# Kernel tuning notes

Measured on AMD Instinct MI355X. Metric: run time of the kernel, lower is better.

Reference implementation:

```python
import jax, jax.numpy as jnp
import numpy as np

B, S = 512, 64
ZD, GD, SK = 256, 16, 512   # vel_z_dim, genre_cond_dim, skel_encode_dim
H = 1024                    # vel_hidden_dim
ND, VC = 9, 4               # n_drum_classes, vel_cond_dim


def _gru(x, h, Wi, Wh, bi, bh):
    # torch.nn.GRUCell math; gates ordered [r, z, n]
    gi = x @ Wi.T + bi
    gh = h @ Wh.T + bh
    i_r, i_z, i_n = jnp.split(gi, 3, axis=-1)
    h_r, h_z, h_n = jnp.split(gh, 3, axis=-1)
    r = jax.nn.sigmoid(i_r + h_r)
    zg = jax.nn.sigmoid(i_z + h_z)
    n = jnp.tanh(i_n + r * h_n)
    return (1.0 - zg) * n + zg * h


def setup_inputs() -> dict:
    key = jax.random.key(0)
    ks = jax.random.split(key, 14)
    rn = lambda k, shp, s: jax.random.normal(k, shp, dtype=jnp.float32) * s
    return dict(
        z=rn(ks[0], (B, ZD), 1.0),
        note_encoded=rn(ks[1], (B, SK), 1.0),
        vel_target=jax.random.uniform(ks[2], (B, S, ND), dtype=jnp.float32),
        note=jax.random.uniform(ks[3], (B, S, ND), dtype=jnp.float32),
        vel_cond=jax.random.uniform(ks[4], (B, S, VC), dtype=jnp.float32),
        genre_cond=rn(ks[5], (B, GD), 1.0),
        W_in=rn(ks[6], (H, ZD + SK + GD), 0.02), b_in=jnp.zeros((H,), jnp.float32),
        W_ih1=rn(ks[7], (3 * H, ND * 2 + VC), 0.05), W_hh1=rn(ks[8], (3 * H, H), 0.02),
        b_ih1=jnp.zeros((3 * H,), jnp.float32), b_hh1=jnp.zeros((3 * H,), jnp.float32),
        W_ih2=rn(ks[9], (3 * H, H), 0.02), W_hh2=rn(ks[10], (3 * H, H), 0.02),
        b_ih2=jnp.zeros((3 * H,), jnp.float32), b_hh2=jnp.zeros((3 * H,), jnp.float32),
        W_out=rn(ks[11], (ND, H), 0.02), b_out=jnp.zeros((ND,), jnp.float32),
        training=0, teacher_forcing_ratio=0,
    )


def reference(z, note_encoded, vel_target, note, vel_cond, genre_cond,
              W_in, b_in, W_ih1, W_hh1, b_ih1, b_hh1,
              W_ih2, W_hh2, b_ih2, b_hh2, W_out, b_out,
              training, teacher_forcing_ratio):
    # eval mode: dropout = identity, teacher forcing never taken
    del vel_target, training, teacher_forcing_ratio
    bsz = z.shape[0]
    zc = jnp.concatenate([z.reshape(bsz, -1), note_encoded, genre_cond], axis=-1)
    h1 = jnp.tanh(zc @ W_in.T + b_in)              # [B, H]
    h2 = jnp.zeros_like(h1)                        # overwritten at step 0
    out0 = jnp.zeros((bsz, W_out.shape[0]), z.dtype)

    def step(carry, xs):
        out, h1, h2 = carry
        i, nt, ct = xs
        inp = jnp.concatenate([out, nt, ct], axis=-1)       # [B, 2*ND+VC]
        h1 = _gru(inp, h1, W_ih1, W_hh1, b_ih1, b_hh1)
        h2 = jnp.where(i == 0, h1, h2)                      # hx[1] = hx[0] at i==0
        h2 = _gru(h1, h2, W_ih2, W_hh2, b_ih2, b_hh2)
        vel = jax.nn.sigmoid(h2 @ W_out.T + b_out)          # [B, ND]
        return (vel, h1, h2), vel

    xs = (jnp.arange(note.shape[1]),
          jnp.transpose(note, (1, 0, 2)),
          jnp.transpose(vel_cond, (1, 0, 2)))
    _, outs = jax.lax.scan(step, (out0, h1, h2), xs)
    return jnp.transpose(outs, (1, 0, 2))                    # [B, S, ND]
```

## Files before the change

kernel.cpp:

```cpp
#include <hip/hip_runtime.h>
#include <hip/hip_bf16.h>

#define HD 1024
#define BB 512
#define SS 64
#define N3 3072
#define NC 9216
#define ND 9
#define VC 4
#define KI 832

typedef __attribute__((ext_vector_type(8))) short bf16x8;
typedef __attribute__((ext_vector_type(4))) float f32x4;

__device__ __forceinline__ ushort f2b(float f) {
    unsigned u = __builtin_bit_cast(unsigned, f);
    u += 0x7fffu + ((u >> 16) & 1u);
    return (ushort)(u >> 16);
}

__device__ __forceinline__ float b2f(ushort u) {
    unsigned x = ((unsigned)u) << 16;
    return __builtin_bit_cast(float, x);
}

__device__ __forceinline__ float sigf(float x) {
    return 1.f / (1.f + __expf(-x));
}

__device__ __forceinline__ void gld_lds16(const void* g, void* l) {
    __builtin_amdgcn_global_load_lds(
        (const __attribute__((address_space(1))) unsigned int*)g,
        (__attribute__((address_space(3))) unsigned int*)l, 16, 0, 0);
}

__global__ __launch_bounds__(256) void prep_w(
    const float* __restrict__ Wih2, const float* __restrict__ Whh1,
    const float* __restrict__ Whh2, ushort* __restrict__ Wcat)
{
    const int row = blockIdx.x;
    const float* src = row < 3072 ? Wih2 + (size_t)row * HD
                     : row < 6144 ? Whh1 + (size_t)(row - 3072) * HD
                                  : Whh2 + (size_t)(row - 6144) * HD;
    const int c = threadIdx.x * 4;
    float4 v = *(const float4*)(src + c);
    ushort4 o;
    o.x = f2b(v.x); o.y = f2b(v.y); o.z = f2b(v.z); o.w = f2b(v.w);
    *(ushort4*)(Wcat + (size_t)row * HD + c) = o;
}

__global__ __launch_bounds__(256) void prep_wt1(
    const float* __restrict__ Wih1, ushort* __restrict__ Wt1b)
{
    const int g = blockIdx.x * 256 + threadIdx.x;
    #pragma unroll
    for (int c = 0; c < 22; ++c)
        Wt1b[c * N3 + g] = f2b(Wih1[(size_t)g * 22 + c]);
}

__global__ __launch_bounds__(256) void prep_acat(
    const float* __restrict__ z, const float* __restrict__ ne,
    const float* __restrict__ gc, ushort* __restrict__ Acat)
{
    const int b = blockIdx.x;
    const int t = threadIdx.x;
    if (t >= 208) return;
    const int c = t * 4;
    float4 v = make_float4(0.f, 0.f, 0.f, 0.f);
    if (c < 256)      v = *(const float4*)(z  + (size_t)b * 256 + c);
    else if (c < 768) v = *(const float4*)(ne + (size_t)b * 512 + (c - 256));
    else if (c < 784) v = *(const float4*)(gc + (size_t)b * 16  + (c - 768));
    ushort4 o;
    o.x = f2b(v.x); o.y = f2b(v.y); o.z = f2b(v.z); o.w = f2b(v.w);
    *(ushort4*)(Acat + (size_t)b * KI + c) = o;
}

__global__ __launch_bounds__(256) void prep_win(
    const float* __restrict__ W_in, ushort* __restrict__ W_inb)
{
    const int r = blockIdx.x;
    const int t = threadIdx.x;
    if (t >= 208) return;
    const int c = t * 4;
    ushort4 o = {0, 0, 0, 0};
    if (c < 784) {
        float4 v = *(const float4*)(W_in + (size_t)r * 784 + c);
        o.x = f2b(v.x); o.y = f2b(v.y); o.z = f2b(v.z); o.w = f2b(v.w);
    }
    *(ushort4*)(W_inb + (size_t)r * KI + c) = o;
}

__global__ __launch_bounds__(256) void k_init(
    const ushort* __restrict__ Acat, const ushort* __restrict__ W_inb,
    const float* __restrict__ b_in, float* __restrict__ h1, ushort* __restrict__ h1b)
{
    __shared__ __align__(16) ushort As[2 * 4096];
    __shared__ __align__(16) ushort Bs[2 * 4096];
    const int t = blockIdx.x;
    const int nt = t >> 3, mt = t & 7;

    const int tid = threadIdx.x;
    const int w = tid >> 6, l = tid & 63;
    const int lr = l >> 3;
    const int sw = ((l & 7) ^ lr) << 3;

    const ushort* Ag0 = Acat + ((size_t)(mt << 6) + 16 * w + lr) * KI + sw;
    const ushort* Ag1 = Ag0 + 8 * KI;
    const ushort* Bg0 = W_inb + ((size_t)(nt << 6) + 16 * w + lr) * KI + sw;
    const ushort* Bg1 = Bg0 + 8 * KI;
    const int o0 = (16 * w) * 64, o1 = (16 * w + 8) * 64;

    gld_lds16(Ag0, As + o0); gld_lds16(Ag1, As + o1);
    gld_lds16(Bg0, Bs + o0); gld_lds16(Bg1, Bs + o1);

    const int wm = (w >> 1) << 5, wn = (w & 1) << 5;
    const int fr = l & 15, fc = l >> 4;
    const int ra0 = wm + fr, ra1 = wm + 16 + fr;
    const int rb0 = wn + fr, rb1 = wn + 16 + fr;

    f32x4 acc[2][2] = {};
    for (int kt = 0; kt < 13; ++kt) {
        const int cb = (kt & 1) << 12;
        __syncthreads();
        if (kt + 1 < 13) {
            const int nb = ((kt + 1) & 1) << 12;
            const int ko = (kt + 1) << 6;
            gld_lds16(Ag0 + ko, As + nb + o0);
            gld_lds16(Ag1 + ko, As + nb + o1);
            gld_lds16(Bg0 + ko, Bs + nb + o0);
            gld_lds16(Bg1 + ko, Bs + nb + o1);
        }
        #pragma unroll
        for (int kk = 0; kk < 2; ++kk) {
            const int c = (kk << 2) + fc;
            bf16x8 a0 = *(const bf16x8*)(As + cb + ra0 * 64 + ((c ^ (ra0 & 7)) << 3));
            bf16x8 a1 = *(const bf16x8*)(As + cb + ra1 * 64 + ((c ^ (ra1 & 7)) << 3));
            bf16x8 b0 = *(const bf16x8*)(Bs + cb + rb0 * 64 + ((c ^ (rb0 & 7)) << 3));
            bf16x8 b1 = *(const bf16x8*)(Bs + cb + rb1 * 64 + ((c ^ (rb1 & 7)) << 3));
            acc[0][0] = __builtin_amdgcn_mfma_f32_16x16x32_bf16(a0, b0, acc[0][0], 0, 0, 0);
            acc[0][1] = __builtin_amdgcn_mfma_f32_16x16x32_bf16(a0, b1, acc[0][1], 0, 0, 0);
            acc[1][0] = __builtin_amdgcn_mfma_f32_16x16x32_bf16(a1, b0, acc[1][0], 0, 0, 0);
            acc[1][1] = __builtin_amdgcn_mfma_f32_16x16x32_bf16(a1, b1, acc[1][1], 0, 0, 0);
        }
    }

    const int row0 = (mt << 6) + wm;
    const int col0 = (nt << 6) + wn + fr;
    const float b0v = b_in[col0], b1v = b_in[col0 + 16];
    #pragma unroll
    for (int i = 0; i < 2; ++i) {
        #pragma unroll
        for (int r = 0; r < 4; ++r) {
            const int row = row0 + i * 16 + fc * 4 + r;
            const float v0 = tanhf(acc[i][0][r] + b0v);
            const float v1 = tanhf(acc[i][1][r] + b1v);
            h1[(size_t)row * HD + col0]       = v0;
            h1b[(size_t)row * HD + col0]      = f2b(v0);
            h1[(size_t)row * HD + col0 + 16]  = v1;
            h1b[(size_t)row * HD + col0 + 16] = f2b(v1);
        }
    }
}

__global__ __launch_bounds__(256) void gemm3(
    const ushort* __restrict__ h1b, const ushort* __restrict__ h2b,
    const ushort* __restrict__ Wcat, ushort* __restrict__ Cbuf, int ntb, int skip48)
{
    __shared__ __align__(16) ushort As[4096];
    __shared__ __align__(16) ushort Ws[4096];

    const int flat = blockIdx.x + (blockIdx.y << 3);
    const int id   = (flat & 7) * gridDim.y + (flat >> 3);
    const int bm   = (id & 7) << 6;
    int nt         = (id >> 3) + ntb;
    if (skip48 && nt >= 48) nt += 48;

    const ushort* Amat = (nt < 96) ? h1b : h2b;
    const ushort* W    = Wcat + (size_t)(nt << 6) * HD;

    const int tid = threadIdx.x;
    const int w   = tid >> 6;
    const int l   = tid & 63;

    const int srow = l >> 3;
    const int sch  = ((l & 7) ^ srow) << 3;
    const ushort* Ag0 = Amat + (size_t)(bm + 16 * w + srow) * HD + sch;
    const ushort* Ag1 = Ag0 + 8 * HD;
    const ushort* Wg0 = W + (size_t)(16 * w + srow) * HD + sch;
    const ushort* Wg1 = Wg0 + 8 * HD;
    ushort* Al0 = As + (16 * w) * 64;
    ushort* Al1 = As + (16 * w + 8) * 64;
    ushort* Wl0 = Ws + (16 * w) * 64;
    ushort* Wl1 = Ws + (16 * w + 8) * 64;

    const int wm = (w >> 1) << 5;
    const int wn = (w & 1) << 5;
    const int fr = l & 15;
    const int fc = l >> 4;

    const int ra0 = wm + fr,  ra1 = wm + 16 + fr;
    const int rb0 = wn + fr,  rb1 = wn + 16 + fr;

    f32x4 acc00 = {0.f,0.f,0.f,0.f}, acc01 = {0.f,0.f,0.f,0.f};
    f32x4 acc10 = {0.f,0.f,0.f,0.f}, acc11 = {0.f,0.f,0.f,0.f};

    for (int kt = 0; kt < 16; ++kt) {
        const int ko = kt << 6;
        __syncthreads();
        gld_lds16(Ag0 + ko, Al0);
        gld_lds16(Ag1 + ko, Al1);
        gld_lds16(Wg0 + ko, Wl0);
        gld_lds16(Wg1 + ko, Wl1);
        __syncthreads();
        #pragma unroll
        for (int kk = 0; kk < 2; ++kk) {
            const int c = (kk << 2) + fc;
            bf16x8 a0 = *(const bf16x8*)(As + ra0 * 64 + ((c ^ (ra0 & 7)) << 3));
            bf16x8 a1 = *(const bf16x8*)(As + ra1 * 64 + ((c ^ (ra1 & 7)) << 3));
            bf16x8 b0 = *(const bf16x8*)(Ws + rb0 * 64 + ((c ^ (rb0 & 7)) << 3));
            bf16x8 b1 = *(const bf16x8*)(Ws + rb1 * 64 + ((c ^ (rb1 & 7)) << 3));
            acc00 = __builtin_amdgcn_mfma_f32_16x16x32_bf16(a0, b0, acc00, 0, 0, 0);
            acc01 = __builtin_amdgcn_mfma_f32_16x16x32_bf16(a0, b1, acc01, 0, 0, 0);
            acc10 = __builtin_amdgcn_mfma_f32_16x16x32_bf16(a1, b0, acc10, 0, 0, 0);
            acc11 = __builtin_amdgcn_mfma_f32_16x16x32_bf16(a1, b1, acc11, 0, 0, 0);
        }
    }

    const int bn = nt << 6;
    ushort* Cw = Cbuf + (size_t)(bm + wm) * NC + bn + wn;
    #pragma unroll
    for (int r = 0; r < 4; ++r) {
        const size_t ro0 = (size_t)(fc * 4 + r) * NC;
        const size_t ro1 = (size_t)(16 + fc * 4 + r) * NC;
        Cw[ro0 + fr]      = f2b(acc00[r]);
        Cw[ro0 + 16 + fr] = f2b(acc01[r]);
        Cw[ro1 + fr]      = f2b(acc10[r]);
        Cw[ro1 + 16 + fr] = f2b(acc11[r]);
    }
}

__global__ __launch_bounds__(1024) void gru1_first(
    const ushort* __restrict__ Cbuf, float* __restrict__ h1, ushort* __restrict__ h1b,
    float* __restrict__ h2, ushort* __restrict__ h2b,
    const float* __restrict__ note, const float* __restrict__ velc,
    const ushort* __restrict__ Wt1b, const float* __restrict__ b_ih1,
    const float* __restrict__ b_hh1)
{
    __shared__ float inp[22];
    const int b = blockIdx.x;
    const int j = threadIdx.x;

    if (j < 22) {
        float v = 0.f;
        if (j >= 9 && j < 18) v = note[(size_t)b * (SS * ND) + (j - 9)];
        else if (j >= 18)     v = velc[(size_t)b * (SS * VC) + (j - 18)];
        inp[j] = v;
    }
    __syncthreads();

    float ir = b_ih1[j], iz = b_ih1[HD + j], inn = b_ih1[2 * HD + j];
    #pragma unroll
    for (int c = 0; c < 22; ++c) {
        const float x = inp[c];
        const ushort* wr = Wt1b + c * N3;
        ir  = fmaf(x, b2f(wr[j]),          ir);
        iz  = fmaf(x, b2f(wr[HD + j]),     iz);
        inn = fmaf(x, b2f(wr[2 * HD + j]), inn);
    }

    const ushort* g = Cbuf + (size_t)b * NC + N3;
    const float hr = b2f(g[j])          + b_hh1[j];
    const float hz = b2f(g[HD + j])     + b_hh1[HD + j];
    const float hn = b2f(g[2 * HD + j]) + b_hh1[2 * HD + j];

    const float rg = sigf(ir + hr);
    const float zg = sigf(iz + hz);
    const float n  = tanhf(inn + rg * hn);
    const float hnew = (1.f - zg) * n + zg * h1[(size_t)b * HD + j];
    const ushort hb = f2b(hnew);
    h1[(size_t)b * HD + j]  = hnew;
    h1b[(size_t)b * HD + j] = hb;
    h2[(size_t)b * HD + j]  = hnew;
    h2b[(size_t)b * HD + j] = hb;
}

__global__ __launch_bounds__(1024) void pw_fused(
    const ushort* __restrict__ Cbuf, float* __restrict__ h1, ushort* __restrict__ h1b,
    float* __restrict__ h2, ushort* __restrict__ h2b,
    const float* __restrict__ note, const float* __restrict__ velc,
    const ushort* __restrict__ Wt1b,
    const float* __restrict__ b_ih1, const float* __restrict__ b_hh1,
    const float* __restrict__ b_ih2, const float* __restrict__ b_hh2,
    const float* __restrict__ W_out, const float* __restrict__ b_out,
    float* __restrict__ dout, int step)
{
    __shared__ float hs[2][HD];
    __shared__ float inp[2][22];
    const int j  = threadIdx.x;
    const int b0 = blockIdx.x * 2;

    if (step + 1 < SS && j < 64) {
        const int r = j >> 5, c = j & 31;
        const int b = b0 + r;
        if (c >= 9 && c < 22)
            inp[r][c] = (c < 18) ? note[(size_t)b * (SS * ND) + (step + 1) * ND + (c - 9)]
                                 : velc[(size_t)b * (SS * VC) + (step + 1) * VC + (c - 18)];
    }

    const float bir = b_ih2[j],          bhr = b_hh2[j];
    const float biz = b_ih2[HD + j],     bhz = b_hh2[HD + j];
    const float bin = b_ih2[2 * HD + j], bhn = b_hh2[2 * HD + j];

    #pragma unroll
    for (int r = 0; r < 2; ++r) {
        const int b = b0 + r;
        const ushort* gi = Cbuf + (size_t)b * NC;
        const ushort* gh = gi + 2 * N3;
        const float ir  = b2f(gi[j]) + bir,          hr = b2f(gh[j]) + bhr;
        const float iz  = b2f(gi[HD + j]) + biz,     hz = b2f(gh[HD + j]) + bhz;
        const float inn = b2f(gi[2 * HD + j]) + bin, hn = b2f(gh[2 * HD + j]) + bhn;
        const float rg = sigf(ir + hr);
        const float zg = sigf(iz + hz);
        const float n  = tanhf(inn + rg * hn);
        const float hnew = (1.f - zg) * n + zg * h2[(size_t)b * HD + j];
        h2[(size_t)b * HD + j]  = hnew;
        h2b[(size_t)b * HD + j] = f2b(hnew);
        hs[r][j] = hnew;
    }
    __syncthreads();

    const int w = j >> 6, t = j & 63;
    {
        const int r = w & 1, b = b0 + r;
        #pragma unroll
        for (int dd = 0; dd < 2; ++dd) {
            const int d = (w >> 1) + dd * 8;
            if (d < ND) {
                float a = 0.f;
                const float* wr = W_out + (size_t)d * HD;
                #pragma unroll
                for (int k = 0; k < HD / 64; ++k)
                    a = fmaf(hs[r][t + k * 64], wr[t + k * 64], a);
                #pragma unroll
                for (int off = 32; off > 0; off >>= 1) a += __shfl_down(a, off);
                if (t == 0) {
                    const float o = sigf(a + b_out[d]);
                    dout[(size_t)b * (SS * ND) + step * ND + d] = o;
                    inp[r][d] = o;
                }
            }
        }
    }
    __syncthreads();

    if (step + 1 < SS) {
        float xir[2], xiz[2], xinn[2];
        #pragma unroll
        for (int r = 0; r < 2; ++r) {
            xir[r] = b_ih1[j]; xiz[r] = b_ih1[HD + j]; xinn[r] = b_ih1[2 * HD + j];
        }
        #pragma unroll
        for (int c = 0; c < 22; ++c) {
            const float w0 = b2f(Wt1b[c * N3 + j]);
            const float w1 = b2f(Wt1b[c * N3 + HD + j]);
            const float w2 = b2f(Wt1b[c * N3 + 2 * HD + j]);
            #pragma unroll
            for (int r = 0; r < 2; ++r) {
                const float x = inp[r][c];
                xir[r]  = fmaf(x, w0, xir[r]);
                xiz[r]  = fmaf(x, w1, xiz[r]);
                xinn[r] = fmaf(x, w2, xinn[r]);
            }
        }
        #pragma unroll
        for (int r = 0; r < 2; ++r) {
            const int b = b0 + r;
            const ushort* g1 = Cbuf + (size_t)b * NC + N3;
            const float hr1 = b2f(g1[j])          + b_hh1[j];
            const float hz1 = b2f(g1[HD + j])     + b_hh1[HD + j];
            const float hn1 = b2f(g1[2 * HD + j]) + b_hh1[2 * HD + j];
            const float rg1 = sigf(xir[r] + hr1);
            const float zg1 = sigf(xiz[r] + hz1);
            const float n1  = tanhf(xinn[r] + rg1 * hn1);
            const float h1new = (1.f - zg1) * n1 + zg1 * h1[(size_t)b * HD + j];
            h1[(size_t)b * HD + j]  = h1new;
            h1b[(size_t)b * HD + j] = f2b(h1new);
        }
    }
}

extern "C" void kernel_launch(void* const* d_in, const int* in_sizes, int n_in,
                              void* d_out, int out_size, void* d_ws, size_t ws_size,
                              hipStream_t stream)
{
    const float* z     = (const float*)d_in[0];
    const float* ne    = (const float*)d_in[1];
    const float* note  = (const float*)d_in[3];
    const float* velc  = (const float*)d_in[4];
    const float* gc    = (const float*)d_in[5];
    const float* W_in  = (const float*)d_in[6];
    const float* b_in  = (const float*)d_in[7];
    const float* W_ih1 = (const float*)d_in[8];
    const float* W_hh1 = (const float*)d_in[9];
    const float* b_ih1 = (const float*)d_in[10];
    const float* b_hh1 = (const float*)d_in[11];
    const float* W_ih2 = (const float*)d_in[12];
    const float* W_hh2 = (const float*)d_in[13];
    const float* b_ih2 = (const float*)d_in[14];
    const float* b_hh2 = (const float*)d_in[15];
    const float* W_out = (const float*)d_in[16];
    const float* b_out = (const float*)d_in[17];
    float* out = (float*)d_out;

    float*  h1   = (float*)d_ws;
    float*  h2   = h1 + BB * HD;
    ushort* Wt1b = (ushort*)(h2 + BB * HD);
    ushort* Cbuf = Wt1b + 22 * N3;
    ushort* h1b  = Cbuf + (size_t)BB * NC;
    ushort* h2b  = h1b + BB * HD;
    ushort* Wcat = h2b + BB * HD;
    ushort* Acat  = Cbuf;
    ushort* W_inb = Acat + (size_t)BB * KI;

    prep_w   <<<dim3(NC), 256, 0, stream>>>(W_ih2, W_hh1, W_hh2, Wcat);
    prep_wt1 <<<dim3(12), 256, 0, stream>>>(W_ih1, Wt1b);
    prep_acat<<<dim3(BB), 256, 0, stream>>>(z, ne, gc, Acat);
    prep_win <<<dim3(HD), 256, 0, stream>>>(W_in, W_inb);

    k_init<<<dim3(128), 256, 0, stream>>>(Acat, W_inb, b_in, h1, h1b);

    gemm3<<<dim3(8, 48), 256, 0, stream>>>(h1b, h2b, Wcat, Cbuf, 48, 0);
    gru1_first<<<dim3(BB), 1024, 0, stream>>>(Cbuf, h1, h1b, h2, h2b,
                                              note, velc, Wt1b, b_ih1, b_hh1);

    for (int s = 0; s < SS; ++s) {
        if (s + 1 < SS)
            gemm3<<<dim3(8, 144), 256, 0, stream>>>(h1b, h2b, Wcat, Cbuf, 0, 0);
        else
            gemm3<<<dim3(8, 96), 256, 0, stream>>>(h1b, h2b, Wcat, Cbuf, 0, 1);
        pw_fused<<<dim3(BB / 2), 1024, 0, stream>>>(Cbuf, h1, h1b, h2, h2b,
                                                    note, velc, Wt1b,
                                                    b_ih1, b_hh1, b_ih2, b_hh2,
                                                    W_out, b_out, out, s);
    }
}
```

Measured before the change: 1.782 ms.

## Split GEMM K dimension in two halves with separate partial output buffers

The per-step GEMM is split along K into two halves, doubling the grid so each block runs 8 K-tiles instead of 16. Each half writes its bf16 partial result to its own buffer (Cbuf or the new Cbuf2), and the pointwise GRU kernels sum the two partials when reading. The aim is more blocks to fill the GPU's compute units during a small per-step GEMM. In exchange it writes and reads twice as much intermediate data, and rounding each partial sum to bf16 adds a little error.

Result: slower. 1.975 ms (+10.8%).

```diff
diff --git a/kernel.cpp b/kernel.cpp
--- a/kernel.cpp
+++ b/kernel.cpp
@@ -164,7 +164,8 @@
 
 __global__ __launch_bounds__(256) void gemm3(
     const ushort* __restrict__ h1b, const ushort* __restrict__ h2b,
-    const ushort* __restrict__ Wcat, ushort* __restrict__ Cbuf, int ntb, int skip48)
+    const ushort* __restrict__ Wcat, ushort* __restrict__ Cbuf,
+    ushort* __restrict__ Cbuf2, int ntb, int skip48)
 {
     __shared__ __align__(16) ushort As[4096];
     __shared__ __align__(16) ushort Ws[4096];
@@ -172,11 +173,14 @@
     const int flat = blockIdx.x + (blockIdx.y << 3);
     const int id   = (flat & 7) * gridDim.y + (flat >> 3);
     const int bm   = (id & 7) << 6;
-    int nt         = (id >> 3) + ntb;
+    const int u    = id >> 3;
+    int nt         = (u >> 1) + ntb;
+    const int kh   = u & 1;
     if (skip48 && nt >= 48) nt += 48;
 
     const ushort* Amat = (nt < 96) ? h1b : h2b;
     const ushort* W    = Wcat + (size_t)(nt << 6) * HD;
+    const int koff     = kh << 9;
 
     const int tid = threadIdx.x;
     const int w   = tid >> 6;
@@ -184,9 +188,9 @@
 
     const int srow = l >> 3;
     const int sch  = ((l & 7) ^ srow) << 3;
-    const ushort* Ag0 = Amat + (size_t)(bm + 16 * w + srow) * HD + sch;
+    const ushort* Ag0 = Amat + (size_t)(bm + 16 * w + srow) * HD + koff + sch;
     const ushort* Ag1 = Ag0 + 8 * HD;
-    const ushort* Wg0 = W + (size_t)(16 * w + srow) * HD + sch;
+    const ushort* Wg0 = W + (size_t)(16 * w + srow) * HD + koff + sch;
     const ushort* Wg1 = Wg0 + 8 * HD;
     ushort* Al0 = As + (16 * w) * 64;
     ushort* Al1 = As + (16 * w + 8) * 64;
@@ -204,7 +208,7 @@
     f32x4 acc00 = {0.f,0.f,0.f,0.f}, acc01 = {0.f,0.f,0.f,0.f};
     f32x4 acc10 = {0.f,0.f,0.f,0.f}, acc11 = {0.f,0.f,0.f,0.f};
 
-    for (int kt = 0; kt < 16; ++kt) {
+    for (int kt = 0; kt < 8; ++kt) {
         const int ko = kt << 6;
         __syncthreads();
         gld_lds16(Ag0 + ko, Al0);
@@ -227,7 +231,7 @@
     }
 
     const int bn = nt << 6;
-    ushort* Cw = Cbuf + (size_t)(bm + wm) * NC + bn + wn;
+    ushort* Cw = (kh ? Cbuf2 : Cbuf) + (size_t)(bm + wm) * NC + bn + wn;
     #pragma unroll
     for (int r = 0; r < 4; ++r) {
         const size_t ro0 = (size_t)(fc * 4 + r) * NC;
@@ -240,7 +244,8 @@
 }
 
 __global__ __launch_bounds__(1024) void gru1_first(
-    const ushort* __restrict__ Cbuf, float* __restrict__ h1, ushort* __restrict__ h1b,
+    const ushort* __restrict__ Ca, const ushort* __restrict__ Cb,
+    float* __restrict__ h1, ushort* __restrict__ h1b,
     float* __restrict__ h2, ushort* __restrict__ h2b,
     const float* __restrict__ note, const float* __restrict__ velc,
     const ushort* __restrict__ Wt1b, const float* __restrict__ b_ih1,
@@ -268,10 +273,11 @@
         inn = fmaf(x, b2f(wr[2 * HD + j]), inn);
     }
 
-    const ushort* g = Cbuf + (size_t)b * NC + N3;
-    const float hr = b2f(g[j])          + b_hh1[j];
-    const float hz = b2f(g[HD + j])     + b_hh1[HD + j];
-    const float hn = b2f(g[2 * HD + j]) + b_hh1[2 * HD + j];
+    const ushort* ga = Ca + (size_t)b * NC + N3;
+    const ushort* gb = Cb + (size_t)b * NC + N3;
+    const float hr = b2f(ga[j])          + b2f(gb[j])          + b_hh1[j];
+    const float hz = b2f(ga[HD + j])     + b2f(gb[HD + j])     + b_hh1[HD + j];
+    const float hn = b2f(ga[2 * HD + j]) + b2f(gb[2 * HD + j]) + b_hh1[2 * HD + j];
 
     const float rg = sigf(ir + hr);
     const float zg = sigf(iz + hz);
@@ -285,7 +291,8 @@
 }
 
 __global__ __launch_bounds__(1024) void pw_fused(
-    const ushort* __restrict__ Cbuf, float* __restrict__ h1, ushort* __restrict__ h1b,
+    const ushort* __restrict__ Ca, const ushort* __restrict__ Cb,
+    float* __restrict__ h1, ushort* __restrict__ h1b,
     float* __restrict__ h2, ushort* __restrict__ h2b,
     const float* __restrict__ note, const float* __restrict__ velc,
     const ushort* __restrict__ Wt1b,
@@ -314,11 +321,16 @@
     #pragma unroll
     for (int r = 0; r < 2; ++r) {
         const int b = b0 + r;
-        const ushort* gi = Cbuf + (size_t)b * NC;
-        const ushort* gh = gi + 2 * N3;
-        const float ir  = b2f(gi[j]) + bir,          hr = b2f(gh[j]) + bhr;
-        const float iz  = b2f(gi[HD + j]) + biz,     hz = b2f(gh[HD + j]) + bhz;
-        const float inn = b2f(gi[2 * HD + j]) + bin, hn = b2f(gh[2 * HD + j]) + bhn;
+        const ushort* gia = Ca + (size_t)b * NC;
+        const ushort* gib = Cb + (size_t)b * NC;
+        const ushort* gha = gia + 2 * N3;
+        const ushort* ghb = gib + 2 * N3;
+        const float ir  = b2f(gia[j]) + b2f(gib[j]) + bir;
+        const float hr  = b2f(gha[j]) + b2f(ghb[j]) + bhr;
+        const float iz  = b2f(gia[HD + j]) + b2f(gib[HD + j]) + biz;
+        const float hz  = b2f(gha[HD + j]) + b2f(ghb[HD + j]) + bhz;
+        const float inn = b2f(gia[2 * HD + j]) + b2f(gib[2 * HD + j]) + bin;
+        const float hn  = b2f(gha[2 * HD + j]) + b2f(ghb[2 * HD + j]) + bhn;
         const float rg = sigf(ir + hr);
         const float zg = sigf(iz + hz);
         const float n  = tanhf(inn + rg * hn);
@@ -375,10 +387,11 @@
         #pragma unroll
         for (int r = 0; r < 2; ++r) {
             const int b = b0 + r;
-            const ushort* g1 = Cbuf + (size_t)b * NC + N3;
-            const float hr1 = b2f(g1[j])          + b_hh1[j];
-            const float hz1 = b2f(g1[HD + j])     + b_hh1[HD + j];
-            const float hn1 = b2f(g1[2 * HD + j]) + b_hh1[2 * HD + j];
+            const ushort* g1a = Ca + (size_t)b * NC + N3;
+            const ushort* g1b = Cb + (size_t)b * NC + N3;
+            const float hr1 = b2f(g1a[j]) + b2f(g1b[j]) + b_hh1[j];
+            const float hz1 = b2f(g1a[HD + j]) + b2f(g1b[HD + j]) + b_hh1[HD + j];
+            const float hn1 = b2f(g1a[2 * HD + j]) + b2f(g1b[2 * HD + j]) + b_hh1[2 * HD + j];
             const float rg1 = sigf(xir[r] + hr1);
             const float zg1 = sigf(xiz[r] + hz1);
             const float n1  = tanhf(xinn[r] + rg1 * hn1);
@@ -412,13 +425,14 @@
     const float* b_out = (const float*)d_in[17];
     float* out = (float*)d_out;
 
-    float*  h1   = (float*)d_ws;
-    float*  h2   = h1 + BB * HD;
-    ushort* Wt1b = (ushort*)(h2 + BB * HD);
-    ushort* Cbuf = Wt1b + 22 * N3;
-    ushort* h1b  = Cbuf + (size_t)BB * NC;
-    ushort* h2b  = h1b + BB * HD;
-    ushort* Wcat = h2b + BB * HD;
+    float*  h1    = (float*)d_ws;
+    float*  h2    = h1 + BB * HD;
+    ushort* Wt1b  = (ushort*)(h2 + BB * HD);
+    ushort* Cbuf  = Wt1b + 22 * N3;
+    ushort* Cbuf2 = Cbuf + (size_t)BB * NC;
+    ushort* h1b   = Cbuf2 + (size_t)BB * NC;
+    ushort* h2b   = h1b + BB * HD;
+    ushort* Wcat  = h2b + BB * HD;
     ushort* Acat  = Cbuf;
     ushort* W_inb = Acat + (size_t)BB * KI;
 
@@ -429,16 +443,16 @@
 
     k_init<<<dim3(128), 256, 0, stream>>>(Acat, W_inb, b_in, h1, h1b);
 
-    gemm3<<<dim3(8, 48), 256, 0, stream>>>(h1b, h2b, Wcat, Cbuf, 48, 0);
-    gru1_first<<<dim3(BB), 1024, 0, stream>>>(Cbuf, h1, h1b, h2, h2b,
+    gemm3<<<dim3(8, 96), 256, 0, stream>>>(h1b, h2b, Wcat, Cbuf, Cbuf2, 48, 0);
+    gru1_first<<<dim3(BB), 1024, 0, stream>>>(Cbuf, Cbuf2, h1, h1b, h2, h2b,
                                               note, velc, Wt1b, b_ih1, b_hh1);
 
     for (int s = 0; s < SS; ++s) {
         if (s + 1 < SS)
-            gemm3<<<dim3(8, 144), 256, 0, stream>>>(h1b, h2b, Wcat, Cbuf, 0, 0);
+            gemm3<<<dim3(8, 288), 256, 0, stream>>>(h1b, h2b, Wcat, Cbuf, Cbuf2, 0, 0);
         else
-            gemm3<<<dim3(8, 96), 256, 0, stream>>>(h1b, h2b, Wcat, Cbuf, 0, 1);
-        pw_fused<<<dim3(BB / 2), 1024, 0, stream>>>(Cbuf, h1, h1b, h2, h2b,
+            gemm3<<<dim3(8, 192), 256, 0, stream>>>(h1b, h2b, Wcat, Cbuf, Cbuf2, 0, 1);
+        pw_fused<<<dim3(BB / 2), 1024, 0, stream>>>(Cbuf, Cbuf2, h1, h1b, h2, h2b,
                                                     note, velc, Wt1b,
                                                     b_ih1, b_hh1, b_ih2, b_hh2,
                                                     W_out, b_out, out, s);
```
